# Kernel tuning notes

Hardware: AMD Instinct MI355X
Metric: run time of the kernel (lower is better)

Reference implementation:

```python
import jax, jax.numpy as jnp
import numpy as np


def setup_inputs() -> dict:
    key = jax.random.key(0)
    ks = jax.random.split(key, 7)
    B, H, W, C = 8, 64, 64, 8
    d = C // 8  # q/k/v channels (= 1 here; forced by the module's broadcast-add)
    x = jax.random.normal(ks[0], (B, H, W, C), dtype=jnp.float32)
    # 1x1 convs == per-pixel linear layers: weight (C, d), bias (d,)
    scale = 1.0 / np.sqrt(C)
    Wq = jax.random.normal(ks[1], (C, d), dtype=jnp.float32) * scale
    bq = jnp.zeros((d,), dtype=jnp.float32)
    Wk = jax.random.normal(ks[2], (C, d), dtype=jnp.float32) * scale
    bk = jnp.zeros((d,), dtype=jnp.float32)
    Wv = jax.random.normal(ks[3], (C, d), dtype=jnp.float32) * scale
    bv = jnp.zeros((d,), dtype=jnp.float32)
    gamma = jnp.float32(0.5)  # nonzero so the attention branch matters
    return {"x": x, "Wq": Wq, "bq": bq, "Wk": Wk, "bk": bk, "Wv": Wv, "bv": bv, "gamma": gamma}


def reference(x, Wq, bq, Wk, bk, Wv, bv, gamma):
    B, H, W, C = x.shape
    N = H * W
    # 1x1 conv projections (NHWC, per-pixel linear)
    q = (jnp.einsum('bhwc,cd->bhwd', x, Wq) + bq).reshape(B, N, -1)  # (B,N,d)
    k = (jnp.einsum('bhwc,cd->bhwd', x, Wk) + bk).reshape(B, N, -1)  # (B,N,d)
    v = (jnp.einsum('bhwc,cd->bhwd', x, Wv) + bv).reshape(B, N, -1)  # (B,N,d)
    # energy[b,i,j] = <q_i, k_j>; NOTE: no 1/sqrt(d) scaling, per source
    energy = jnp.einsum('bnd,bmd->bnm', q, k)  # (B,N,N)
    attention = jax.nn.softmax(energy, axis=-1)
    # out[b,i,d] = sum_j attention[b,i,j] * v[b,j,d]
    out = jnp.einsum('bnm,bmd->bnd', attention, v).reshape(B, H, W, -1)  # (B,H,W,d)
    # gamma-scaled residual; d==1 so out broadcasts against C channels
    y = out * gamma + x
    return (y, attention)
```

## Files before the change

kernel.cpp:

```cpp
#include <hip/hip_runtime.h>
#include <math.h>

#define NPIX 4096
#define CCH 8
#define BLK 256
#define NW   (BLK/64)
#define RPW  8
#define TILE (NW*RPW)
#define L2E 1.44269504088896340736f

typedef float floatx4 __attribute__((ext_vector_type(4)));

__global__ __launch_bounds__(256) void kv_project(
    const float* __restrict__ x,
    const float* __restrict__ Wk, const float* __restrict__ bk,
    const float* __restrict__ Wv, const float* __restrict__ bv,
    float* __restrict__ kbuf, float* __restrict__ vbuf)
{
    const int b = blockIdx.y;
    const int j = blockIdx.x * 256 + threadIdx.x;

    float wk[CCH], wv[CCH];
#pragma unroll
    for (int c = 0; c < CCH; ++c) { wk[c] = Wk[c]; wv[c] = Wv[c]; }
    const float bkv = bk[0], bvv = bv[0];

    const float4* xp = reinterpret_cast<const float4*>(x + ((size_t)b * NPIX + j) * CCH);
    float4 x0 = xp[0];
    float4 x1 = xp[1];
    float kj = bkv;
    kj = fmaf(x0.x, wk[0], kj); kj = fmaf(x0.y, wk[1], kj);
    kj = fmaf(x0.z, wk[2], kj); kj = fmaf(x0.w, wk[3], kj);
    kj = fmaf(x1.x, wk[4], kj); kj = fmaf(x1.y, wk[5], kj);
    kj = fmaf(x1.z, wk[6], kj); kj = fmaf(x1.w, wk[7], kj);
    float vj = bvv;
    vj = fmaf(x0.x, wv[0], vj); vj = fmaf(x0.y, wv[1], vj);
    vj = fmaf(x0.z, wv[2], vj); vj = fmaf(x0.w, wv[3], vj);
    vj = fmaf(x1.x, wv[4], vj); vj = fmaf(x1.y, wv[5], vj);
    vj = fmaf(x1.z, wv[6], vj); vj = fmaf(x1.w, wv[7], vj);

    kbuf[(size_t)b * NPIX + j] = kj;
    vbuf[(size_t)b * NPIX + j] = vj;
}

__global__ __launch_bounds__(BLK) void attn_main(
    const float* __restrict__ x,
    const float* __restrict__ Wq, const float* __restrict__ bq,
    const float* __restrict__ gamma_p,
    const float* __restrict__ kbuf, const float* __restrict__ vbuf,
    float* __restrict__ y, float* __restrict__ attn)
{
    __shared__ float ks[NPIX];
    __shared__ float vs[NPIX];
    __shared__ float kred[2][NW];

    const int b = blockIdx.y;
    const int rowbase = blockIdx.x * TILE;
    const int tid = threadIdx.x;
    const int wid = tid >> 6;
    const int lane = tid & 63;

    float wq[CCH];
#pragma unroll
    for (int c = 0; c < CCH; ++c) wq[c] = Wq[c];
    const float bqv = bq[0];
    const float gamma = gamma_p[0];

    const float* xb = x + (size_t)b * NPIX * CCH;
    const float4* kb4 = reinterpret_cast<const float4*>(kbuf + (size_t)b * NPIX);
    const float4* vb4 = reinterpret_cast<const float4*>(vbuf + (size_t)b * NPIX);

    float kmx = -INFINITY, kmn = INFINITY;
#pragma unroll
    for (int i = 0; i < 4; ++i) {
        const int idx = tid + i * 256;
        float4 kk = kb4[idx];
        float4 vv = vb4[idx];
        *reinterpret_cast<float4*>(&ks[idx * 4]) = kk;
        *reinterpret_cast<float4*>(&vs[idx * 4]) = vv;
        kmx = fmaxf(kmx, fmaxf(fmaxf(kk.x, kk.y), fmaxf(kk.z, kk.w)));
        kmn = fminf(kmn, fminf(fminf(kk.x, kk.y), fminf(kk.z, kk.w)));
    }
#pragma unroll
    for (int off = 32; off > 0; off >>= 1) {
        kmx = fmaxf(kmx, __shfl_xor(kmx, off));
        kmn = fminf(kmn, __shfl_xor(kmn, off));
    }
    if (lane == 0) { kred[0][wid] = kmx; kred[1][wid] = kmn; }
    __syncthreads();
    kmx = fmaxf(fmaxf(kred[0][0], kred[0][1]), fmaxf(kred[0][2], kred[0][3]));
    kmn = fminf(fminf(kred[1][0], kred[1][1]), fminf(kred[1][2], kred[1][3]));

    const int r8 = lane & 7;
    const int irow0 = rowbase + wid * RPW;
    const float4* xq = reinterpret_cast<const float4*>(xb + (size_t)(irow0 + r8) * CCH);
    float4 a0 = xq[0];
    float4 a1 = xq[1];
    float q = bqv;
    q = fmaf(a0.x, wq[0], q); q = fmaf(a0.y, wq[1], q);
    q = fmaf(a0.z, wq[2], q); q = fmaf(a0.w, wq[3], q);
    q = fmaf(a1.x, wq[4], q); q = fmaf(a1.y, wq[5], q);
    q = fmaf(a1.z, wq[6], q); q = fmaf(a1.w, wq[7], q);
    const float q2v = q * L2E;
    const float m2v = q2v * ((q >= 0.f) ? kmx : kmn);

    const float4* ks4 = reinterpret_cast<const float4*>(ks);
    const float4* vs4 = reinterpret_cast<const float4*>(vs);
    float* ap_base = attn + ((size_t)b * NPIX + irow0) * (size_t)NPIX;

    for (int rr = 0; rr < RPW; ++rr) {
        const float q2r = __shfl(q2v, rr);
        const float m2r = __shfl(m2v, rr);

        float s = 0.f, o = 0.f;
#pragma unroll
        for (int g = 0; g < 16; ++g) {
            float4 kk = ks4[lane + g * 64];
            float4 vv = vs4[lane + g * 64];
            float e0 = exp2f(fmaf(q2r, kk.x, -m2r));
            float e1 = exp2f(fmaf(q2r, kk.y, -m2r));
            float e2 = exp2f(fmaf(q2r, kk.z, -m2r));
            float e3 = exp2f(fmaf(q2r, kk.w, -m2r));
            s += (e0 + e1) + (e2 + e3);
            o += fmaf(e0, vv.x, e1 * vv.y) + fmaf(e2, vv.z, e3 * vv.w);
        }
#pragma unroll
        for (int off = 32; off > 0; off >>= 1) {
            s += __shfl_xor(s, off);
            o += __shfl_xor(o, off);
        }
        const float invs = 1.0f / s;

        const int i = irow0 + rr;
        if (lane < 2) {
            const float og = o * invs * gamma;
            const float4 xv = *reinterpret_cast<const float4*>(xb + (size_t)i * CCH + lane * 4);
            float4 yv = { og + xv.x, og + xv.y, og + xv.z, og + xv.w };
            *reinterpret_cast<float4*>(y + ((size_t)b * NPIX + i) * CCH + lane * 4) = yv;
        }

        float* ap = ap_base + (size_t)rr * NPIX;
#pragma unroll
        for (int g = 0; g < 16; ++g) {
            float4 kk = ks4[lane + g * 64];
            floatx4 e;
            e.x = exp2f(fmaf(q2r, kk.x, -m2r)) * invs;
            e.y = exp2f(fmaf(q2r, kk.y, -m2r)) * invs;
            e.z = exp2f(fmaf(q2r, kk.z, -m2r)) * invs;
            e.w = exp2f(fmaf(q2r, kk.w, -m2r)) * invs;
            __builtin_nontemporal_store(e, reinterpret_cast<floatx4*>(ap + (lane + g * 64) * 4));
        }
    }
}

#define ROWS 32
#define NP   (BLK/ROWS)
#define SEG  (NPIX/NP)

__global__ __launch_bounds__(BLK) void attn_fused(
    const float* __restrict__ x,
    const float* __restrict__ Wq, const float* __restrict__ bq,
    const float* __restrict__ Wk, const float* __restrict__ bk,
    const float* __restrict__ Wv, const float* __restrict__ bv,
    const float* __restrict__ gamma_p,
    float* __restrict__ y, float* __restrict__ attn)
{
    __shared__ float ks[NPIX];
    __shared__ float vs[NPIX];
    __shared__ float qrow[ROWS];
    __shared__ float crow[ROWS];
    __shared__ float spart[NP][ROWS];
    __shared__ float opart[NP][ROWS];
    __shared__ float kred[2][NW];

    const int b = blockIdx.y;
    const int rowbase = blockIdx.x * ROWS;
    const int tid = threadIdx.x;
    const int wid = tid >> 6;
    const int lane = tid & 63;

    float wq[CCH], wk[CCH], wv[CCH];
#pragma unroll
    for (int c = 0; c < CCH; ++c) { wq[c] = Wq[c]; wk[c] = Wk[c]; wv[c] = Wv[c]; }
    const float bqv = bq[0], bkv = bk[0], bvv = bv[0];
    const float gamma = gamma_p[0];
    const float* xb = x + (size_t)b * NPIX * CCH;

    float kmx = -INFINITY, kmn = INFINITY;
    for (int j = tid; j < NPIX; j += BLK) {
        const float4* xp = reinterpret_cast<const float4*>(xb + (size_t)j * CCH);
        float4 x0 = xp[0];
        float4 x1 = xp[1];
        float kj = bkv;
        kj = fmaf(x0.x, wk[0], kj); kj = fmaf(x0.y, wk[1], kj);
        kj = fmaf(x0.z, wk[2], kj); kj = fmaf(x0.w, wk[3], kj);
        kj = fmaf(x1.x, wk[4], kj); kj = fmaf(x1.y, wk[5], kj);
        kj = fmaf(x1.z, wk[6], kj); kj = fmaf(x1.w, wk[7], kj);
        float vj = bvv;
        vj = fmaf(x0.x, wv[0], vj); vj = fmaf(x0.y, wv[1], vj);
        vj = fmaf(x0.z, wv[2], vj); vj = fmaf(x0.w, wv[3], vj);
        vj = fmaf(x1.x, wv[4], vj); vj = fmaf(x1.y, wv[5], vj);
        vj = fmaf(x1.z, wv[6], vj); vj = fmaf(x1.w, wv[7], vj);
        ks[j] = kj; vs[j] = vj;
        kmx = fmaxf(kmx, kj); kmn = fminf(kmn, kj);
    }
#pragma unroll
    for (int off = 32; off > 0; off >>= 1) {
        kmx = fmaxf(kmx, __shfl_xor(kmx, off));
        kmn = fminf(kmn, __shfl_xor(kmn, off));
    }
    if (lane == 0) { kred[0][wid] = kmx; kred[1][wid] = kmn; }
    __syncthreads();
    kmx = fmaxf(fmaxf(kred[0][0], kred[0][1]), fmaxf(kred[0][2], kred[0][3]));
    kmn = fminf(fminf(kred[1][0], kred[1][1]), fminf(kred[1][2], kred[1][3]));

    const int r = tid & (ROWS - 1);
    const int p = tid >> 5;
    const int i = rowbase + r;
    const float4* xq = reinterpret_cast<const float4*>(xb + (size_t)i * CCH);
    float4 a0 = xq[0];
    float4 a1 = xq[1];
    float q = bqv;
    q = fmaf(a0.x, wq[0], q); q = fmaf(a0.y, wq[1], q);
    q = fmaf(a0.z, wq[2], q); q = fmaf(a0.w, wq[3], q);
    q = fmaf(a1.x, wq[4], q); q = fmaf(a1.y, wq[5], q);
    q = fmaf(a1.z, wq[6], q); q = fmaf(a1.w, wq[7], q);
    const float q2 = q * L2E;
    const float m2 = q2 * ((q >= 0.f) ? kmx : kmn);

    float s0 = 0.f, s1 = 0.f, s2 = 0.f, s3 = 0.f;
    float o0 = 0.f, o1 = 0.f, o2 = 0.f, o3 = 0.f;
    const int j0 = p * SEG;
    for (int j = j0; j < j0 + SEG; j += 4) {
        float4 kk = *reinterpret_cast<const float4*>(&ks[j]);
        float4 vv = *reinterpret_cast<const float4*>(&vs[j]);
        float e0 = exp2f(fmaf(q2, kk.x, -m2));
        float e1 = exp2f(fmaf(q2, kk.y, -m2));
        float e2 = exp2f(fmaf(q2, kk.z, -m2));
        float e3 = exp2f(fmaf(q2, kk.w, -m2));
        s0 += e0; s1 += e1; s2 += e2; s3 += e3;
        o0 = fmaf(e0, vv.x, o0);
        o1 = fmaf(e1, vv.y, o1);
        o2 = fmaf(e2, vv.z, o2);
        o3 = fmaf(e3, vv.w, o3);
    }
    spart[p][r] = (s0 + s1) + (s2 + s3);
    opart[p][r] = (o0 + o1) + (o2 + o3);
    __syncthreads();

    if (tid < ROWS) {
        float s = 0.f, o = 0.f;
#pragma unroll
        for (int pp = 0; pp < NP; ++pp) { s += spart[pp][tid]; o += opart[pp][tid]; }
        const float og = (o / s) * gamma;
        const int i2 = rowbase + tid;
        const float4* xr = reinterpret_cast<const float4*>(xb + (size_t)i2 * CCH);
        float4 b0 = xr[0];
        float4 b1 = xr[1];
        float* yp = y + ((size_t)b * NPIX + i2) * CCH;
        float4 y0 = { og + b0.x, og + b0.y, og + b0.z, og + b0.w };
        float4 y1 = { og + b1.x, og + b1.y, og + b1.z, og + b1.w };
        *reinterpret_cast<float4*>(yp) = y0;
        *reinterpret_cast<float4*>(yp + 4) = y1;
        qrow[tid] = q2;
        crow[tid] = m2 + log2f(s);
    }
    __syncthreads();

    const int j4 = tid * 4;
    float4 kk0 = *reinterpret_cast<const float4*>(&ks[j4]);
    float4 kk1 = *reinterpret_cast<const float4*>(&ks[j4 + 1024]);
    float4 kk2 = *reinterpret_cast<const float4*>(&ks[j4 + 2048]);
    float4 kk3 = *reinterpret_cast<const float4*>(&ks[j4 + 3072]);

    float* ap0 = attn + ((size_t)b * NPIX + rowbase) * (size_t)NPIX;
    for (int rr = 0; rr < ROWS; ++rr) {
        const float qr = qrow[rr];
        const float cr = crow[rr];
        float* ap = ap0 + (size_t)rr * NPIX;
        floatx4 e0, e1, e2, e3;
        e0.x = exp2f(fmaf(qr, kk0.x, -cr)); e0.y = exp2f(fmaf(qr, kk0.y, -cr));
        e0.z = exp2f(fmaf(qr, kk0.z, -cr)); e0.w = exp2f(fmaf(qr, kk0.w, -cr));
        e1.x = exp2f(fmaf(qr, kk1.x, -cr)); e1.y = exp2f(fmaf(qr, kk1.y, -cr));
        e1.z = exp2f(fmaf(qr, kk1.z, -cr)); e1.w = exp2f(fmaf(qr, kk1.w, -cr));
        e2.x = exp2f(fmaf(qr, kk2.x, -cr)); e2.y = exp2f(fmaf(qr, kk2.y, -cr));
        e2.z = exp2f(fmaf(qr, kk2.z, -cr)); e2.w = exp2f(fmaf(qr, kk2.w, -cr));
        e3.x = exp2f(fmaf(qr, kk3.x, -cr)); e3.y = exp2f(fmaf(qr, kk3.y, -cr));
        e3.z = exp2f(fmaf(qr, kk3.z, -cr)); e3.w = exp2f(fmaf(qr, kk3.w, -cr));
        __builtin_nontemporal_store(e0, reinterpret_cast<floatx4*>(&ap[j4]));
        __builtin_nontemporal_store(e1, reinterpret_cast<floatx4*>(&ap[j4 + 1024]));
        __builtin_nontemporal_store(e2, reinterpret_cast<floatx4*>(&ap[j4 + 2048]));
        __builtin_nontemporal_store(e3, reinterpret_cast<floatx4*>(&ap[j4 + 3072]));
    }
}

extern "C" void kernel_launch(void* const* d_in, const int* in_sizes, int n_in,
                              void* d_out, int out_size, void* d_ws, size_t ws_size,
                              hipStream_t stream) {
    const float* x   = (const float*)d_in[0];
    const float* Wq  = (const float*)d_in[1];
    const float* bq  = (const float*)d_in[2];
    const float* Wk  = (const float*)d_in[3];
    const float* bk  = (const float*)d_in[4];
    const float* Wv  = (const float*)d_in[5];
    const float* bv  = (const float*)d_in[6];
    const float* gm  = (const float*)d_in[7];

    const int B = in_sizes[0] / (NPIX * CCH);
    float* y    = (float*)d_out;
    float* attn = y + (size_t)B * NPIX * CCH;

    const size_t kv_bytes = (size_t)B * NPIX * 2 * sizeof(float);
    if (ws_size >= kv_bytes) {
        float* kbuf = (float*)d_ws;
        float* vbuf = kbuf + (size_t)B * NPIX;
        dim3 gridA(NPIX / 256, B);
        kv_project<<<gridA, 256, 0, stream>>>(x, Wk, bk, Wv, bv, kbuf, vbuf);
        dim3 gridB(NPIX / TILE, B);
        attn_main<<<gridB, BLK, 0, stream>>>(x, Wq, bq, gm, kbuf, vbuf, y, attn);
    } else {
        dim3 grid(NPIX / ROWS, B);
        attn_fused<<<grid, BLK, 0, stream>>>(x, Wq, bq, Wk, bk, Wv, bv, gm, y, attn);
    }
}
```

Baseline: 113.5 us.

## Software-pipeline row passes and fold softmax normalizer into exponent offset

Restructures the per-warp row loop so each iteration writes the normalized attention row for the previous row while computing the sum and weighted-v reduction for the next row, sharing the K/V shared-memory loads. The 1/s multiply is removed by folding log2(s) into the exponent offset, so each stored value is a single exp2. The aim is to overlap the store-heavy write pass with the reduction pass and cut LDS reads and multiplies. It adds a log2 per row and small rounding differences, and raises register pressure from the interleaved loops.

```diff
diff --git a/kernel.cpp b/kernel.cpp
--- a/kernel.cpp
+++ b/kernel.cpp
@@ -108,19 +108,18 @@
     const float4* vs4 = reinterpret_cast<const float4*>(vs);
     float* ap_base = attn + ((size_t)b * NPIX + irow0) * (size_t)NPIX;
 
-    for (int rr = 0; rr < RPW; ++rr) {
-        const float q2r = __shfl(q2v, rr);
-        const float m2r = __shfl(m2v, rr);
-
+    float q2c = __shfl(q2v, 0);
+    float m2c = __shfl(m2v, 0);
+    {
         float s = 0.f, o = 0.f;
 #pragma unroll
         for (int g = 0; g < 16; ++g) {
             float4 kk = ks4[lane + g * 64];
             float4 vv = vs4[lane + g * 64];
-            float e0 = exp2f(fmaf(q2r, kk.x, -m2r));
-            float e1 = exp2f(fmaf(q2r, kk.y, -m2r));
-            float e2 = exp2f(fmaf(q2r, kk.z, -m2r));
-            float e3 = exp2f(fmaf(q2r, kk.w, -m2r));
+            float e0 = exp2f(fmaf(q2c, kk.x, -m2c));
+            float e1 = exp2f(fmaf(q2c, kk.y, -m2c));
+            float e2 = exp2f(fmaf(q2c, kk.z, -m2c));
+            float e3 = exp2f(fmaf(q2c, kk.w, -m2c));
             s += (e0 + e1) + (e2 + e3);
             o += fmaf(e0, vv.x, e1 * vv.y) + fmaf(e2, vv.z, e3 * vv.w);
         }
@@ -129,25 +128,63 @@
             s += __shfl_xor(s, off);
             o += __shfl_xor(o, off);
         }
-        const float invs = 1.0f / s;
-
-        const int i = irow0 + rr;
         if (lane < 2) {
-            const float og = o * invs * gamma;
+            const float og = (o / s) * gamma;
+            const float4 xv = *reinterpret_cast<const float4*>(xb + (size_t)irow0 * CCH + lane * 4);
+            float4 yv = { og + xv.x, og + xv.y, og + xv.z, og + xv.w };
+            *reinterpret_cast<float4*>(y + ((size_t)b * NPIX + irow0) * CCH + lane * 4) = yv;
+        }
+        m2c = m2c + log2f(s);
+    }
+
+    for (int r = 1; r < RPW; ++r) {
+        const float q2n = __shfl(q2v, r);
+        const float m2n = __shfl(m2v, r);
+        float sn = 0.f, on = 0.f;
+        float* ap = ap_base + (size_t)(r - 1) * NPIX;
+#pragma unroll
+        for (int g = 0; g < 16; ++g) {
+            float4 kk = ks4[lane + g * 64];
+            float4 vv = vs4[lane + g * 64];
+            floatx4 e;
+            e.x = exp2f(fmaf(q2c, kk.x, -m2c));
+            e.y = exp2f(fmaf(q2c, kk.y, -m2c));
+            e.z = exp2f(fmaf(q2c, kk.z, -m2c));
+            e.w = exp2f(fmaf(q2c, kk.w, -m2c));
+            __builtin_nontemporal_store(e, reinterpret_cast<floatx4*>(ap + (lane + g * 64) * 4));
+            float n0 = exp2f(fmaf(q2n, kk.x, -m2n));
+            float n1 = exp2f(fmaf(q2n, kk.y, -m2n));
+            float n2 = exp2f(fmaf(q2n, kk.z, -m2n));
+            float n3 = exp2f(fmaf(q2n, kk.w, -m2n));
+            sn += (n0 + n1) + (n2 + n3);
+            on += fmaf(n0, vv.x, n1 * vv.y) + fmaf(n2, vv.z, n3 * vv.w);
+        }
+#pragma unroll
+        for (int off = 32; off > 0; off >>= 1) {
+            sn += __shfl_xor(sn, off);
+            on += __shfl_xor(on, off);
+        }
+        const int i = irow0 + r;
+        if (lane < 2) {
+            const float og = (on / sn) * gamma;
             const float4 xv = *reinterpret_cast<const float4*>(xb + (size_t)i * CCH + lane * 4);
             float4 yv = { og + xv.x, og + xv.y, og + xv.z, og + xv.w };
             *reinterpret_cast<float4*>(y + ((size_t)b * NPIX + i) * CCH + lane * 4) = yv;
         }
-
-        float* ap = ap_base + (size_t)rr * NPIX;
+        q2c = q2n;
+        m2c = m2n + log2f(sn);
+    }
+
+    {
+        float* ap = ap_base + (size_t)(RPW - 1) * NPIX;
 #pragma unroll
         for (int g = 0; g < 16; ++g) {
             float4 kk = ks4[lane + g * 64];
             floatx4 e;
-            e.x = exp2f(fmaf(q2r, kk.x, -m2r)) * invs;
-            e.y = exp2f(fmaf(q2r, kk.y, -m2r)) * invs;
-            e.z = exp2f(fmaf(q2r, kk.z, -m2r)) * invs;
-            e.w = exp2f(fmaf(q2r, kk.w, -m2r)) * invs;
+            e.x = exp2f(fmaf(q2c, kk.x, -m2c));
+            e.y = exp2f(fmaf(q2c, kk.y, -m2c));
+            e.z = exp2f(fmaf(q2c, kk.z, -m2c));
+            e.w = exp2f(fmaf(q2c, kk.w, -m2c));
             __builtin_nontemporal_store(e, reinterpret_cast<floatx4*>(ap + (lane + g * 64) * 4));
         }
     }
```

Result: slower. 117.4 us (+3.4%).
